# Kernel optimization log

Hardware: AMD Instinct MI355X
Metric: run time of the kernel (lower is better)

Reference implementation:

```python
import jax, jax.numpy as jnp
import numpy as np

B = 64      # batch
N = 2048    # map obstacle points
S = 4       # num_step (distinct planner per step)
A = 8       # num_anchor_per_step
H = 256     # size_middle
L = 2       # lstm num_layers
LOC = 3     # len_info_loc (x, y, theta)
WH = 64     # map_width_half == map_height_half
INTERVAL = 0.2
CIN, COUT, K, STRIDE, PAD = 4, 8, 5, 2, 2
O = (2 * WH + 2 * PAD - K) // STRIDE + 1  # 64
DLM = (2.0, 2.0, 0.5)   # delta_limit_mean
DLV = 0.1               # delta_limit_var


def setup_inputs() -> dict:
    key = jax.random.key(0)
    ks = jax.random.split(key, 16)

    def w(k, shape, fan_in):
        return jax.random.normal(k, shape, jnp.float32) / np.sqrt(fan_in)

    return {
        "inp_start_point": jax.random.normal(ks[0], (B, 1, LOC), jnp.float32),
        "map_pts": jax.random.uniform(ks[1], (2, N), jnp.float32, -12.8, 12.8),
        "ela_w1": w(ks[2], (S, H, LOC), LOC),
        "ela_w2": w(ks[3], (S, H, H), H),
        "conv_w": w(ks[4], (S, COUT, CIN, K, K), CIN * K * K),
        "elm_w1": w(ks[5], (S, H, O * O), O * O),
        "elm_w2": w(ks[6], (S, H, H), H),
        "ebl_w1": w(ks[7], (S, H, 2 * H), 2 * H),
        "ebl_w2": w(ks[8], (S, H, H), H),
        "lstm_wih": w(ks[9], (S, L, 4 * H, H), H),
        "lstm_whh": w(ks[10], (S, L, 4 * H, H), H),
        "dm_w1": w(ks[11], (S, H, H), H),
        "dm_w2": w(ks[12], (S, LOC, H), H),
        "dv_w1": w(ks[13], (S, H, H), H),
        "dv_w2": w(ks[14], (S, LOC, H), H),
    }


def _ogm(map_pts, anchor):
    """points2ogm + cal_map_last: rotate/translate global map into ego frame,
    nearest-bin argmin, scatter 1s into a [B, 128, 128] occupancy grid."""
    rel = map_pts.T[None, :, :] - anchor[:, :, 0:2]        # [B,N,2]
    m = jnp.swapaxes(rel, 1, 2)                            # [B,2,N]
    th = anchor[:, 0, 2]                                   # [B]
    c, s = jnp.cos(th), jnp.sin(th)
    rot = jnp.stack([jnp.stack([c, s], -1), jnp.stack([-s, c], -1)], axis=1)  # [B,2,2]
    pts = rot @ m                                          # [B,2,N]
    x, y = pts[:, 0], pts[:, 1]                            # [B,N]
    lim = WH * INTERVAL
    out = (jnp.abs(x) > lim) | (jnp.abs(y) > lim)
    x = jnp.where(out, 0.0, x)
    y = jnp.where(out, 0.0, y)
    centers = (jnp.arange(-WH, WH, dtype=jnp.float32) + 0.5) * INTERVAL  # [2*WH]
    x_id = jnp.argmin(jnp.abs(centers[None, None, :] - x[:, :, None]), axis=2)  # [B,N]
    y_id = jnp.argmin(jnp.abs(centers[None, None, :] - y[:, :, None]), axis=2)  # [B,N]
    b_idx = jnp.arange(B)[:, None]
    return jnp.zeros((B, 2 * WH, 2 * WH), jnp.float32).at[b_idx, x_id, y_id].set(1.0)


def _conv(x, w):
    return jax.lax.conv_general_dilated(
        x, w, (STRIDE, STRIDE), [(PAD, PAD), (PAD, PAD)],
        dimension_numbers=("NCHW", "OIHW", "NCHW"))


def _ln(x):  # LayerNorm, no affine, eps=1e-5
    mu = jnp.mean(x, axis=-1, keepdims=True)
    v = jnp.var(x, axis=-1, keepdims=True)
    return (x - mu) / jnp.sqrt(v + 1e-5)


def _mlp2(x, w1, w2):  # Linear -> ReLU -> Linear, no bias
    return jax.nn.relu(x @ w1.T) @ w2.T


def reference(inp_start_point, map_pts, ela_w1, ela_w2, conv_w, elm_w1, elm_w2,
              ebl_w1, ebl_w2, lstm_wih, lstm_whh, dm_w1, dm_w2, dv_w1, dv_w2):
    dlm = jnp.array(DLM, jnp.float32)
    anchor = inp_start_point                       # [B,1,3]
    var_last = jnp.ones_like(anchor) * 0.01
    pre_mean, pre_var = [], []
    for st in range(S):
        dm_list, dv_list = [anchor], [var_last]
        h = jnp.ones((L, B, H), jnp.float32)
        c = jnp.ones((L, B, H), jnp.float32)
        for _ in range(A - 1):
            ela = _mlp2(anchor, ela_w1[st], ela_w2[st])                 # [B,1,H]
            ogm = jax.lax.stop_gradient(_ogm(map_pts, anchor))          # [B,128,128]
            xin = jnp.broadcast_to(ogm[:, None], (B, CIN, 2 * WH, 2 * WH))
            conv = jnp.tanh(_conv(xin, conv_w[st])).sum(axis=1)         # [B,O,O]
            elm = _mlp2(conv.reshape(B, 1, O * O), elm_w1[st], elm_w2[st])  # [B,1,H]
            ebl = _mlp2(jnp.concatenate([ela, elm], axis=2), ebl_w1[st], ebl_w2[st])  # [B,1,H]
            # single-timestep multi-layer LSTM, no bias, gate order i,f,g,o
            x = ebl[:, 0]                                               # [B,H]
            for l in range(L):
                g = x @ lstm_wih[st, l].T + h[l] @ lstm_whh[st, l].T    # [B,4H]
                gi, gf, gg, go = jnp.split(g, 4, axis=-1)
                cl = jax.nn.sigmoid(gf) * c[l] + jax.nn.sigmoid(gi) * jnp.tanh(gg)
                hl = jax.nn.sigmoid(go) * jnp.tanh(cl)
                h = h.at[l].set(hl)
                c = c.at[l].set(cl)
                x = hl
            mn = _ln(x[:, None]) + ebl                                  # [B,1,H]
            r = jax.nn.relu(mn)
            anchors_now = jnp.tanh(_mlp2(r, dm_w1[st], dm_w2[st])) * dlm + anchor
            var_now = jax.nn.sigmoid(_mlp2(r, dv_w1[st], dv_w2[st])) * DLV
            anchor, var_last = anchors_now, var_now
            dm_list.append(anchors_now)
            dv_list.append(var_now)
        pre_mean.append(jnp.concatenate(dm_list, axis=1))               # [B,A,3]
        pre_var.append(jnp.concatenate(dv_list, axis=1))
    pre_mean = jnp.stack(pre_mean, axis=1)                              # [B,S,A,3]
    pre_var = jnp.stack(pre_var, axis=1)
    return pre_mean, pre_var
```

## Files before the change

kernel.cpp:

```cpp
#include <hip/hip_runtime.h>

#define WGSZ 1024
#define NWG  256

namespace {
constexpr int kN = 2048, kH = 256, kGW = 512;
constexpr size_t OFF_ITM = 16384;
constexpr size_t OFF_W0  = OFF_ITM + 64 * 4096;
constexpr size_t TO_ELA2 = 0;
constexpr size_t TO_ELM1 = 262144;
constexpr size_t TO_ELM2 = 4456448;
constexpr size_t TO_EBL1 = 4718592;
constexpr size_t TO_EBL2 = 5242880;
constexpr size_t TO_DM1  = 5505024;
constexpr size_t TO_DV1  = 5767168;
constexpr size_t TO_WIH  = 6029312;
constexpr size_t TO_WHH  = 8126464;
constexpr size_t W_FLOATS = 10223616;
constexpr size_t WS_FULL  = OFF_W0 + W_FLOATS;
constexpr int I_CAT = 0, I_ELMH = 512, I_EBLH = 768, I_EBLO = 1024,
              I_G0 = 1280, I_G1 = 2304, I_DMH = 3328, I_DVH = 3584;
}

__device__ __forceinline__ int bin_idx(float v) {
  float t = fmaf(v, 5.0f, 63.5f);
  int i0 = (int)floorf(t);
  int c0 = i0 - 1; c0 = c0 < 0 ? 0 : (c0 > 127 ? 127 : c0);
  int c1 = i0;     c1 = c1 < 0 ? 0 : (c1 > 127 ? 127 : c1);
  int c2 = i0 + 1; c2 = c2 < 0 ? 0 : (c2 > 127 ? 127 : c2);
  float d0 = fabsf(__fmul_rn(__fadd_rn((float)(c0 - 64), 0.5f), 0.2f) - v);
  float d1 = fabsf(__fmul_rn(__fadd_rn((float)(c1 - 64), 0.5f), 0.2f) - v);
  float d2 = fabsf(__fmul_rn(__fadd_rn((float)(c2 - 64), 0.5f), 0.2f) - v);
  int best = c0; float bd = d0;
  if (d1 < bd) { bd = d1; best = c1; }
  if (d2 < bd) { bd = d2; best = c2; }
  return best;
}

__device__ __forceinline__ float np_pw128(const float* a) {
  float r0=a[0],r1=a[1],r2=a[2],r3=a[3],r4=a[4],r5=a[5],r6=a[6],r7=a[7];
  for (int i = 8; i < 128; i += 8) {
    r0=__fadd_rn(r0,a[i+0]); r1=__fadd_rn(r1,a[i+1]);
    r2=__fadd_rn(r2,a[i+2]); r3=__fadd_rn(r3,a[i+3]);
    r4=__fadd_rn(r4,a[i+4]); r5=__fadd_rn(r5,a[i+5]);
    r6=__fadd_rn(r6,a[i+6]); r7=__fadd_rn(r7,a[i+7]);
  }
  return __fadd_rn(__fadd_rn(__fadd_rn(r0,r1),__fadd_rn(r2,r3)),
                   __fadd_rn(__fadd_rn(r4,r5),__fadd_rn(r6,r7)));
}
__device__ __forceinline__ float np_sum256(const float* a) {
  return __fadd_rn(np_pw128(a), np_pw128(a + 128));
}

__device__ __forceinline__ float sig_np(float x) {
  return __fdiv_rn(1.0f, __fadd_rn(1.0f, expf(-x)));
}

__device__ __forceinline__ void fma4(float& aa, float4 w, float4 v) {
  aa = fmaf(w.x, v.x, aa); aa = fmaf(w.y, v.y, aa);
  aa = fmaf(w.z, v.z, aa); aa = fmaf(w.w, v.w, aa);
}

__device__ __forceinline__ void gl_lds(const float4* g, float4* l) {
  __builtin_amdgcn_global_load_lds(
      (__attribute__((address_space(1))) void*)g,
      (__attribute__((address_space(3))) void*)l, 16, 0, 0);
}

__device__ __forceinline__ void bat_bar(unsigned* cnt, int tid) {
  __syncthreads();
  if (tid == 0) {
    __threadfence();
    __hip_atomic_fetch_add(cnt, 1u, __ATOMIC_RELEASE, __HIP_MEMORY_SCOPE_AGENT);
    while (__hip_atomic_load(cnt, __ATOMIC_ACQUIRE,
                             __HIP_MEMORY_SCOPE_AGENT) < 4u)
      __builtin_amdgcn_s_sleep(1);
  }
  __syncthreads();
}

#define MV_STAGE(CI, BI)                                                       \
  do {                                                                         \
    float4* dst = wb[BI] + wid * 64;                                           \
    const int cs0 = (CI) * CK4;                                                \
    if (wT) gl_lds(wT + (size_t)(cs0 + k4l) * Rg + G0 + sub * 64 + lane, dst); \
    else    gl_lds(wO + (size_t)(G0 + sub * 64 + lane) * k4o + cs0 + k4l, dst);\
  } while (0)

#define MV_COMP(BI, CI)                                                        \
  do {                                                                         \
    if (tid < RW) {                                                            \
      const float4* sb = wb[BI];                                               \
      const int cc0 = (CI) * CK4;                                              \
      for (int kk = 0; kk < CK4; ++kk)                                         \
        fma4(acc, sb[kk * RW + tid], x4[cc0 + kk]);                            \
    }                                                                          \
  } while (0)

template<int RW>
__device__ float mv_split(float4 (*wb)[1024], const float4* wT,
                          const float4* wO, int k4o, int Rg, int K4, int G0,
                          const float4* x4, int tid, float acc0) {
  constexpr int RW64 = RW / 64;
  constexpr int CK4  = 16 / RW64;
  const int C = K4 / CK4;
  const int wid = tid >> 6, lane = tid & 63;
  const int k4l = wid / RW64, sub = wid - k4l * RW64;
  float acc = acc0;
  MV_STAGE(0, 0);
  MV_STAGE(1, 1);
  MV_STAGE(2, 2);
  MV_STAGE(3, 3);
  int c = 0, cbuf = 0, sbuf = 4;
  for (; c + 4 < C; ++c) {
    MV_STAGE(c + 4, sbuf);
    asm volatile("s_waitcnt vmcnt(4)" ::: "memory");
    __builtin_amdgcn_s_barrier();
    MV_COMP(cbuf, c);
    sbuf = (sbuf == 5) ? 0 : sbuf + 1;
    cbuf = (cbuf == 5) ? 0 : cbuf + 1;
  }
  asm volatile("s_waitcnt vmcnt(3)" ::: "memory");
  __builtin_amdgcn_s_barrier();
  MV_COMP(cbuf, c);
  cbuf = (cbuf == 5) ? 0 : cbuf + 1; ++c;
  asm volatile("s_waitcnt vmcnt(2)" ::: "memory");
  __builtin_amdgcn_s_barrier();
  MV_COMP(cbuf, c);
  cbuf = (cbuf == 5) ? 0 : cbuf + 1; ++c;
  asm volatile("s_waitcnt vmcnt(1)" ::: "memory");
  __builtin_amdgcn_s_barrier();
  MV_COMP(cbuf, c);
  cbuf = (cbuf == 5) ? 0 : cbuf + 1; ++c;
  asm volatile("s_waitcnt vmcnt(0)" ::: "memory");
  __builtin_amdgcn_s_barrier();
  MV_COMP(cbuf, c);
  __syncthreads();
  return acc;
}

struct TransArgs {
  const float* src[9];
  float*       dst[9];
  int          n4[9];
  int          rmask[9];
  int          rshift[9];
  int          K[9];
};

__global__ void prep_kernel(TransArgs a, unsigned* bar, int nmat) {
  const int gtid = blockIdx.x * blockDim.x + threadIdx.x;
  const int gsz  = gridDim.x * blockDim.x;
  for (int i = gtid; i < 16384; i += gsz) bar[i] = 0u;
  for (int m = 0; m < nmat; ++m) {
    const float* __restrict__ src = a.src[m];
    float4* __restrict__ dst = (float4*)a.dst[m];
    const int n = a.n4[m], rm = a.rmask[m], rs = a.rshift[m], K = a.K[m];
    for (int i = gtid; i < n; i += gsz) {
      const int r = i & rm, k4 = i >> rs;
      const float* s = src + (size_t)r * K + (size_t)k4 * 4;
      float4 v; v.x = s[0]; v.y = s[1]; v.z = s[2]; v.w = s[3];
      dst[i] = v;
    }
  }
}

__global__ __launch_bounds__(WGSZ, 4) void planner_kernel(
    const float* __restrict__ inp_start, const float* __restrict__ map_pts,
    const float* __restrict__ ela_w1, const float* __restrict__ ela_w2,
    const float* __restrict__ conv_w, const float* __restrict__ elm_w1,
    const float* __restrict__ elm_w2, const float* __restrict__ ebl_w1,
    const float* __restrict__ ebl_w2, const float* __restrict__ lstm_wih,
    const float* __restrict__ lstm_whh, const float* __restrict__ dm_w1,
    const float* __restrict__ dm_w2, const float* __restrict__ dv_w1,
    const float* __restrict__ dv_w2, float* __restrict__ ws,
    int useT, float* __restrict__ g_out) {
  const int b   = blockIdx.x >> 2;
  const int g   = blockIdx.x & 3;
  const int tid = threadIdx.x;
  float* itm = ws + OFF_ITM + (size_t)b * 4096;
  unsigned* barp = (unsigned*)ws + (size_t)b * 256;
  const float4* wsW = (const float4*)(ws + OFF_W0);

  __shared__ __align__(16) float4 s_wbuf[6][1024];
  __shared__ unsigned s_mask[kGW];
  __shared__ __align__(16) float s_conv[4096];
  __shared__ __align__(16) float s_cw[800];
  __shared__ __align__(16) float s_elah[kH];
  __shared__ __align__(16) float s_xa[512];
  __shared__ __align__(16) float s_eblo[kH];
  __shared__ __align__(16) float s_r[kH];
  __shared__ __align__(16) float s_gate[1024];
  __shared__ __align__(16) float s_h0[kH], s_c0[kH], s_h1[kH], s_c1[kH];
  __shared__ __align__(16) float s_ones[kH];
  __shared__ __align__(16) float s_tmp[512];
  __shared__ __align__(16) float s_hw[1536];
  __shared__ float s_anchor[3], s_cs[2], s_g6[6];
  __shared__ float s_mu, s_den;

  if (tid == 0) {
    float a2 = inp_start[b * 3 + 2];
    s_anchor[0] = inp_start[b * 3 + 0];
    s_anchor[1] = inp_start[b * 3 + 1];
    s_anchor[2] = a2;
    s_cs[0] = (float)cos((double)a2);
    s_cs[1] = (float)sin((double)a2);
  }
  if (tid < kH) s_ones[tid] = 1.0f;
  if (g == 0 && tid < 3) {
    g_out[b * 96 + tid] = inp_start[b * 3 + tid];
    g_out[6144 + b * 96 + tid] = 0.01f;
  }
  __syncthreads();

  int sidx = 0;
  for (int k = 0; k < 28; ++k) {
    const int st = k / 7, a = k % 7;
    const bool a0f = (a == 0);

    if (tid < kGW) s_mask[tid] = 0u;
    if (tid < 800) s_cw[tid] = conv_w[st * 800 + tid];
    if (tid < kH) {
      const float* w1r = ela_w1 + (st * kH + tid) * 3;
      float h = fmaf(s_anchor[2], w1r[2],
                fmaf(s_anchor[1], w1r[1], __fmul_rn(s_anchor[0], w1r[0])));
      s_elah[tid] = fmaxf(h, 0.0f);
    }
    if (tid < 1536)
      s_hw[tid] = (tid < 768) ? dm_w2[st * 768 + tid]
                              : dv_w2[st * 768 + tid - 768];
    __syncthreads();

    {
      float ax = s_anchor[0], ay = s_anchor[1], cc = s_cs[0], ss = s_cs[1];
      for (int n = tid; n < kN; n += WGSZ) {
        float mx = __fadd_rn(map_pts[n],      -ax);
        float my = __fadd_rn(map_pts[kN + n], -ay);
        float px = fmaf(ss, my, __fmul_rn(cc, mx));
        float py = fmaf(cc, my, -__fmul_rn(ss, mx));
        bool outb = (fabsf(px) > 12.8f) || (fabsf(py) > 12.8f);
        px = outb ? 0.0f : px;
        py = outb ? 0.0f : py;
        int xi = bin_idx(px), yi = bin_idx(py);
        atomicOr(&s_mask[xi * 4 + (yi >> 5)], 1u << (yi & 31));
      }
    }
    __syncthreads();

    for (int q = 0; q < 4; ++q) {
      const int p = tid + (q << 10);
      const int oy = p >> 6, ox = p & 63;
      unsigned occ = 0u;
      for (int ky = 0; ky < 5; ++ky) {
        const int y = 2 * oy - 2 + ky;
        if ((unsigned)y >= 128u) continue;
        const unsigned* row = &s_mask[y * 4];
        for (int kx = 0; kx < 5; ++kx) {
          const int x = 2 * ox - 2 + kx;
          if ((unsigned)x >= 128u) continue;
          if ((row[x >> 5] >> (x & 31)) & 1u) occ |= 1u << (ky * 5 + kx);
        }
      }
      float csum = 0.0f;
      if (occ != 0u) {
        for (int o = 0; o < 8; ++o) {
          float acc = 0.0f;
          const float* wo = s_cw + o * 100;
          for (int ci = 0; ci < 4; ++ci) {
            const float* wc = wo + ci * 25;
            #pragma unroll
            for (int t = 0; t < 25; ++t)
              acc = __fadd_rn(acc, ((occ >> t) & 1u) ? wc[t] : 0.0f);
          }
          float th = tanhf(acc);
          csum = (o == 0) ? th : __fadd_rn(csum, th);
        }
      }
      s_conv[p] = csum;
    }
    __syncthreads();

    const int G64 = st * 256 + g * 64;

    {
      float acc = mv_split<64>(s_wbuf, useT ? wsW + TO_ELA2 / 4 : nullptr,
                               (const float4*)ela_w2, 64, 1024, 64, G64,
                               (const float4*)s_elah, tid, 0.0f);
      if (tid < 64) itm[I_CAT + g * 64 + tid] = acc;
      acc = mv_split<64>(s_wbuf, useT ? wsW + TO_ELM1 / 4 : nullptr,
                         (const float4*)elm_w1, 1024, 1024, 1024, G64,
                         (const float4*)s_conv, tid, 0.0f);
      if (tid < 64) itm[I_ELMH + g * 64 + tid] = fmaxf(acc, 0.0f);
    }
    bat_bar(barp + sidx, tid); ++sidx;

    if (tid < kH) s_xa[tid] = itm[I_ELMH + tid];
    __syncthreads();
    {
      float acc = mv_split<64>(s_wbuf, useT ? wsW + TO_ELM2 / 4 : nullptr,
                               (const float4*)elm_w2, 64, 1024, 64, G64,
                               (const float4*)s_xa, tid, 0.0f);
      if (tid < 64) itm[I_CAT + 256 + g * 64 + tid] = acc;
    }
    bat_bar(barp + sidx, tid); ++sidx;

    if (tid < 512) s_xa[tid] = itm[I_CAT + tid];
    __syncthreads();
    {
      float acc = mv_split<64>(s_wbuf, useT ? wsW + TO_EBL1 / 4 : nullptr,
                               (const float4*)ebl_w1, 128, 1024, 128, G64,
                               (const float4*)s_xa, tid, 0.0f);
      if (tid < 64) itm[I_EBLH + g * 64 + tid] = fmaxf(acc, 0.0f);
    }
    bat_bar(barp + sidx, tid); ++sidx;

    if (tid < kH) s_xa[tid] = itm[I_EBLH + tid];
    __syncthreads();
    {
      float acc = mv_split<64>(s_wbuf, useT ? wsW + TO_EBL2 / 4 : nullptr,
                               (const float4*)ebl_w2, 64, 1024, 64, G64,
                               (const float4*)s_xa, tid, 0.0f);
      if (tid < 64) itm[I_EBLO + g * 64 + tid] = acc;
    }
    bat_bar(barp + sidx, tid); ++sidx;

    if (tid < kH) s_eblo[tid] = itm[I_EBLO + tid];
    __syncthreads();
    for (int l = 0; l < 2; ++l) {
      const int rowb = (st * 2 + l) * 1024 + g * 256;
      const float* xe = (l == 0) ? s_eblo : s_h0;
      const float* xh = a0f ? s_ones : ((l == 0) ? s_h0 : s_h1);
      float accA = mv_split<256>(s_wbuf, useT ? wsW + TO_WIH / 4 : nullptr,
                                 (const float4*)lstm_wih, 64, 8192, 64, rowb,
                                 (const float4*)xe, tid, 0.0f);
      float accB = mv_split<256>(s_wbuf, useT ? wsW + TO_WHH / 4 : nullptr,
                                 (const float4*)lstm_whh, 64, 8192, 64, rowb,
                                 (const float4*)xh, tid, 0.0f);
      const int IG = (l == 0) ? I_G0 : I_G1;
      if (tid < kH) itm[IG + g * 256 + tid] = __fadd_rn(accA, accB);
      bat_bar(barp + sidx, tid); ++sidx;
      s_gate[tid] = itm[IG + tid];
      __syncthreads();
      if (tid < kH) {
        float gi = s_gate[tid], gf = s_gate[256 + tid];
        float gg = s_gate[512 + tid], go = s_gate[768 + tid];
        float* sc = (l == 0) ? s_c0 : s_c1;
        float* sh = (l == 0) ? s_h0 : s_h1;
        float cprev = a0f ? 1.0f : sc[tid];
        float cl = __fadd_rn(__fmul_rn(sig_np(gf), cprev),
                             __fmul_rn(sig_np(gi), tanhf(gg)));
        float hl = __fmul_rn(sig_np(go), tanhf(cl));
        sc[tid] = cl; sh[tid] = hl;
      }
      __syncthreads();
    }

    if (tid == 0) s_mu = __fdiv_rn(np_sum256(s_h1), 256.0f);
    __syncthreads();
    if (tid < kH) {
      float d = __fadd_rn(s_h1[tid], -s_mu);
      s_tmp[tid] = d;
      s_tmp[256 + tid] = __fmul_rn(d, d);
    }
    __syncthreads();
    if (tid == 0) {
      float v = __fdiv_rn(np_sum256(s_tmp + 256), 256.0f);
      s_den = __fsqrt_rn(__fadd_rn(v, 1e-5f));
    }
    __syncthreads();
    if (tid < kH) {
      float r = __fadd_rn(__fdiv_rn(s_tmp[tid], s_den), s_eblo[tid]);
      s_r[tid] = fmaxf(r, 0.0f);
    }
    __syncthreads();

    {
      float acc = mv_split<64>(s_wbuf, useT ? wsW + TO_DM1 / 4 : nullptr,
                               (const float4*)dm_w1, 64, 1024, 64, G64,
                               (const float4*)s_r, tid, 0.0f);
      if (tid < 64) itm[I_DMH + g * 64 + tid] = fmaxf(acc, 0.0f);
      acc = mv_split<64>(s_wbuf, useT ? wsW + TO_DV1 / 4 : nullptr,
                         (const float4*)dv_w1, 64, 1024, 64, G64,
                         (const float4*)s_r, tid, 0.0f);
      if (tid < 64) itm[I_DVH + g * 64 + tid] = fmaxf(acc, 0.0f);
    }
    bat_bar(barp + sidx, tid); ++sidx;

    if (tid < 512)
      s_xa[tid] = (tid < 256) ? itm[I_DMH + tid] : itm[I_DVH + tid - 256];
    __syncthreads();
    if (tid < 6) {
      const int d = tid % 3; const bool isv = tid >= 3;
      const float4* w4 = (const float4*)(s_hw + (isv ? 768 : 0) + d * 256);
      const float4* xx = (const float4*)(isv ? s_xa + 256 : s_xa);
      float acc = 0.0f;
      for (int i = 0; i < 64; ++i) fma4(acc, w4[i], xx[i]);
      s_g6[tid] = acc;
    }
    __syncthreads();
    if (tid == 0) {
      const float dlmf[3] = {2.0f, 2.0f, 0.5f};
      for (int d = 0; d < 3; ++d) {
        float avn = __fadd_rn(s_anchor[d], __fmul_rn(tanhf(s_g6[d]), dlmf[d]));
        float vvn = __fmul_rn(sig_np(s_g6[3 + d]), 0.1f);
        s_anchor[d] = avn;
        if (g == 0) {
          int o = ((b * 4 + st) * 8 + (a + 1)) * 3 + d;
          g_out[o] = avn;
          g_out[6144 + o] = vvn;
          if (a == 6 && st < 3) {
            int o2 = ((b * 4 + st + 1) * 8 + 0) * 3 + d;
            g_out[o2] = avn;
            g_out[6144 + o2] = vvn;
          }
        }
      }
      s_cs[0] = (float)cos((double)s_anchor[2]);
      s_cs[1] = (float)sin((double)s_anchor[2]);
    }
    __syncthreads();
  }
}

extern "C" void kernel_launch(void* const* d_in, const int* in_sizes, int n_in,
                              void* d_out, int out_size, void* d_ws, size_t ws_size,
                              hipStream_t stream) {
  (void)in_sizes; (void)n_in; (void)out_size;
  float* wsf = (float*)d_ws;
  const int useT = (ws_size >= WS_FULL * sizeof(float)) ? 1 : 0;

  TransArgs ta;
  const float* srcs[9] = {
      (const float*)d_in[3],  (const float*)d_in[5],  (const float*)d_in[6],
      (const float*)d_in[7],  (const float*)d_in[8],  (const float*)d_in[11],
      (const float*)d_in[13], (const float*)d_in[9],  (const float*)d_in[10]};
  float* w0 = wsf + OFF_W0;
  float* dsts[9] = {w0 + TO_ELA2, w0 + TO_ELM1, w0 + TO_ELM2, w0 + TO_EBL1,
                    w0 + TO_EBL2, w0 + TO_DM1,  w0 + TO_DV1,  w0 + TO_WIH,
                    w0 + TO_WHH};
  const int n4s[9] = {65536, 1048576, 65536, 131072, 65536, 65536, 65536,
                      524288, 524288};
  const int rms[9] = {1023, 1023, 1023, 1023, 1023, 1023, 1023, 8191, 8191};
  const int rss[9] = {10, 10, 10, 10, 10, 10, 10, 13, 13};
  const int Ks[9]  = {256, 4096, 256, 512, 256, 256, 256, 256, 256};
  for (int m = 0; m < 9; ++m) {
    ta.src[m] = srcs[m]; ta.dst[m] = dsts[m]; ta.n4[m] = n4s[m];
    ta.rmask[m] = rms[m]; ta.rshift[m] = rss[m]; ta.K[m] = Ks[m];
  }
  prep_kernel<<<dim3(1024), dim3(256), 0, stream>>>(
      ta, (unsigned*)d_ws, useT ? 9 : 0);

  planner_kernel<<<dim3(NWG), dim3(WGSZ), 0, stream>>>(
      (const float*)d_in[0],  (const float*)d_in[1],  (const float*)d_in[2],
      (const float*)d_in[3],  (const float*)d_in[4],  (const float*)d_in[5],
      (const float*)d_in[6],  (const float*)d_in[7],  (const float*)d_in[8],
      (const float*)d_in[9],  (const float*)d_in[10], (const float*)d_in[11],
      (const float*)d_in[12], (const float*)d_in[13], (const float*)d_in[14],
      wsf, useT, (float*)d_out);
}
```

Baseline: 8.289 ms.

## Batch eight samples per workgroup team to reuse weight tiles across batch

Restructures the persistent planner kernel from 4 workgroups per batch element (256 WGs) to 64 workgroups organized as 8 teams of 8, each team handling 8 batch elements together. Each WG now computes a 32-row slice for all 8 batch elements, so every weight tile staged into LDS is reused 8 times instead of once, cutting global weight traffic. Intermediates move to global workspace with per-team barriers over 8 WGs, and activations are staged in padded LDS layouts. The trade-offs are more barriers and global round trips per stage, less parallelism, and a simpler double-buffered pipeline replacing the 6-deep one.

```diff
diff --git a/kernel.cpp b/kernel.cpp
--- a/kernel.cpp
+++ b/kernel.cpp
@@ -1,12 +1,21 @@
 #include <hip/hip_runtime.h>
 
 #define WGSZ 1024
-#define NWG  256
+#define NWG  64
 
 namespace {
-constexpr int kN = 2048, kH = 256, kGW = 512;
-constexpr size_t OFF_ITM = 16384;
-constexpr size_t OFF_W0  = OFF_ITM + 64 * 4096;
+constexpr int kN = 2048;
+constexpr size_t OFF_CONV = 2048;
+constexpr size_t OFF_ELAH = 264192;
+constexpr size_t OFF_CAT  = 280576;
+constexpr size_t OFF_ELMH = 313344;
+constexpr size_t OFF_EBLH = 329728;
+constexpr size_t OFF_EBLO = 346112;
+constexpr size_t OFF_H0   = 362496;
+constexpr size_t OFF_H1   = 395264;
+constexpr size_t OFF_DMH  = 428032;
+constexpr size_t OFF_DVH  = 444416;
+constexpr size_t OFF_W0   = 460800;
 constexpr size_t TO_ELA2 = 0;
 constexpr size_t TO_ELM1 = 262144;
 constexpr size_t TO_ELM2 = 4456448;
@@ -18,8 +27,7 @@
 constexpr size_t TO_WHH  = 8126464;
 constexpr size_t W_FLOATS = 10223616;
 constexpr size_t WS_FULL  = OFF_W0 + W_FLOATS;
-constexpr int I_CAT = 0, I_ELMH = 512, I_EBLH = 768, I_EBLO = 1024,
-              I_G0 = 1280, I_G1 = 2304, I_DMH = 3328, I_DVH = 3584;
+constexpr int XP = 9;
 }
 
 __device__ __forceinline__ int bin_idx(float v) {
@@ -37,28 +45,45 @@
   return best;
 }
 
-__device__ __forceinline__ float np_pw128(const float* a) {
-  float r0=a[0],r1=a[1],r2=a[2],r3=a[3],r4=a[4],r5=a[5],r6=a[6],r7=a[7];
-  for (int i = 8; i < 128; i += 8) {
-    r0=__fadd_rn(r0,a[i+0]); r1=__fadd_rn(r1,a[i+1]);
-    r2=__fadd_rn(r2,a[i+2]); r3=__fadd_rn(r3,a[i+3]);
-    r4=__fadd_rn(r4,a[i+4]); r5=__fadd_rn(r5,a[i+5]);
-    r6=__fadd_rn(r6,a[i+6]); r7=__fadd_rn(r7,a[i+7]);
-  }
-  return __fadd_rn(__fadd_rn(__fadd_rn(r0,r1),__fadd_rn(r2,r3)),
-                   __fadd_rn(__fadd_rn(r4,r5),__fadd_rn(r6,r7)));
-}
-__device__ __forceinline__ float np_sum256(const float* a) {
-  return __fadd_rn(np_pw128(a), np_pw128(a + 128));
-}
-
 __device__ __forceinline__ float sig_np(float x) {
   return __fdiv_rn(1.0f, __fadd_rn(1.0f, expf(-x)));
 }
+__device__ __forceinline__ float sqf(float x) { return __fmul_rn(x, x); }
 
 __device__ __forceinline__ void fma4(float& aa, float4 w, float4 v) {
   aa = fmaf(w.x, v.x, aa); aa = fmaf(w.y, v.y, aa);
   aa = fmaf(w.z, v.z, aa); aa = fmaf(w.w, v.w, aa);
+}
+
+__device__ __forceinline__ float np_pw128_s9(const float* a) {
+  float r0=a[0*XP],r1=a[1*XP],r2=a[2*XP],r3=a[3*XP];
+  float r4=a[4*XP],r5=a[5*XP],r6=a[6*XP],r7=a[7*XP];
+  for (int i = 8; i < 128; i += 8) {
+    r0=__fadd_rn(r0,a[(i+0)*XP]); r1=__fadd_rn(r1,a[(i+1)*XP]);
+    r2=__fadd_rn(r2,a[(i+2)*XP]); r3=__fadd_rn(r3,a[(i+3)*XP]);
+    r4=__fadd_rn(r4,a[(i+4)*XP]); r5=__fadd_rn(r5,a[(i+5)*XP]);
+    r6=__fadd_rn(r6,a[(i+6)*XP]); r7=__fadd_rn(r7,a[(i+7)*XP]);
+  }
+  return __fadd_rn(__fadd_rn(__fadd_rn(r0,r1),__fadd_rn(r2,r3)),
+                   __fadd_rn(__fadd_rn(r4,r5),__fadd_rn(r6,r7)));
+}
+__device__ __forceinline__ float np_sum256_s9(const float* a) {
+  return __fadd_rn(np_pw128_s9(a), np_pw128_s9(a + 128 * XP));
+}
+__device__ __forceinline__ float np_pw128_sq_s9(const float* a) {
+  float r0=sqf(a[0*XP]),r1=sqf(a[1*XP]),r2=sqf(a[2*XP]),r3=sqf(a[3*XP]);
+  float r4=sqf(a[4*XP]),r5=sqf(a[5*XP]),r6=sqf(a[6*XP]),r7=sqf(a[7*XP]);
+  for (int i = 8; i < 128; i += 8) {
+    r0=__fadd_rn(r0,sqf(a[(i+0)*XP])); r1=__fadd_rn(r1,sqf(a[(i+1)*XP]));
+    r2=__fadd_rn(r2,sqf(a[(i+2)*XP])); r3=__fadd_rn(r3,sqf(a[(i+3)*XP]));
+    r4=__fadd_rn(r4,sqf(a[(i+4)*XP])); r5=__fadd_rn(r5,sqf(a[(i+5)*XP]));
+    r6=__fadd_rn(r6,sqf(a[(i+6)*XP])); r7=__fadd_rn(r7,sqf(a[(i+7)*XP]));
+  }
+  return __fadd_rn(__fadd_rn(__fadd_rn(r0,r1),__fadd_rn(r2,r3)),
+                   __fadd_rn(__fadd_rn(r4,r5),__fadd_rn(r6,r7)));
+}
+__device__ __forceinline__ float np_sum256_sq_s9(const float* a) {
+  return __fadd_rn(np_pw128_sq_s9(a), np_pw128_sq_s9(a + 128 * XP));
 }
 
 __device__ __forceinline__ void gl_lds(const float4* g, float4* l) {
@@ -73,70 +98,103 @@
     __threadfence();
     __hip_atomic_fetch_add(cnt, 1u, __ATOMIC_RELEASE, __HIP_MEMORY_SCOPE_AGENT);
     while (__hip_atomic_load(cnt, __ATOMIC_ACQUIRE,
-                             __HIP_MEMORY_SCOPE_AGENT) < 4u)
+                             __HIP_MEMORY_SCOPE_AGENT) < 8u)
       __builtin_amdgcn_s_sleep(1);
   }
   __syncthreads();
 }
 
-#define MV_STAGE(CI, BI)                                                       \
-  do {                                                                         \
-    float4* dst = wb[BI] + wid * 64;                                           \
-    const int cs0 = (CI) * CK4;                                                \
-    if (wT) gl_lds(wT + (size_t)(cs0 + k4l) * Rg + G0 + sub * 64 + lane, dst); \
-    else    gl_lds(wO + (size_t)(G0 + sub * 64 + lane) * k4o + cs0 + k4l, dst);\
-  } while (0)
-
-#define MV_COMP(BI, CI)                                                        \
-  do {                                                                         \
-    if (tid < RW) {                                                            \
-      const float4* sb = wb[BI];                                               \
-      const int cc0 = (CI) * CK4;                                              \
-      for (int kk = 0; kk < CK4; ++kk)                                         \
-        fma4(acc, sb[kk * RW + tid], x4[cc0 + kk]);                            \
-    }                                                                          \
-  } while (0)
-
-template<int RW>
-__device__ float mv_split(float4 (*wb)[1024], const float4* wT,
-                          const float4* wO, int k4o, int Rg, int K4, int G0,
-                          const float4* x4, int tid, float acc0) {
-  constexpr int RW64 = RW / 64;
-  constexpr int CK4  = 16 / RW64;
-  const int C = K4 / CK4;
+__device__ __forceinline__ void stage_x(float* xl, const float* src0,
+                                        int stride, int L, int tid) {
+  const int bat = tid >> 7, i = tid & 127;
+  const float* sp = src0 + (size_t)bat * stride;
+  for (int k = i; k < L; k += 128) xl[k * XP + bat] = sp[k];
+}
+
+__device__ float mv32(float4 (*wb)[1024], const float4* wT, const float4* wO,
+                      int k4o, int Rg, int R0g, int k4base, int C,
+                      const float* xl, int tid, float acc) {
   const int wid = tid >> 6, lane = tid & 63;
-  const int k4l = wid / RW64, sub = wid - k4l * RW64;
-  float acc = acc0;
-  MV_STAGE(0, 0);
-  MV_STAGE(1, 1);
-  MV_STAGE(2, 2);
-  MV_STAGE(3, 3);
-  int c = 0, cbuf = 0, sbuf = 4;
-  for (; c + 4 < C; ++c) {
-    MV_STAGE(c + 4, sbuf);
-    asm volatile("s_waitcnt vmcnt(4)" ::: "memory");
-    __builtin_amdgcn_s_barrier();
-    MV_COMP(cbuf, c);
-    sbuf = (sbuf == 5) ? 0 : sbuf + 1;
-    cbuf = (cbuf == 5) ? 0 : cbuf + 1;
-  }
-  asm volatile("s_waitcnt vmcnt(3)" ::: "memory");
-  __builtin_amdgcn_s_barrier();
-  MV_COMP(cbuf, c);
-  cbuf = (cbuf == 5) ? 0 : cbuf + 1; ++c;
-  asm volatile("s_waitcnt vmcnt(2)" ::: "memory");
-  __builtin_amdgcn_s_barrier();
-  MV_COMP(cbuf, c);
-  cbuf = (cbuf == 5) ? 0 : cbuf + 1; ++c;
-  asm volatile("s_waitcnt vmcnt(1)" ::: "memory");
-  __builtin_amdgcn_s_barrier();
-  MV_COMP(cbuf, c);
-  cbuf = (cbuf == 5) ? 0 : cbuf + 1; ++c;
-  asm volatile("s_waitcnt vmcnt(0)" ::: "memory");
-  __builtin_amdgcn_s_barrier();
-  MV_COMP(cbuf, c);
+  const int kkw = (wid << 1) + (lane >> 5), rw = lane & 31;
+  {
+    const int k4g = k4base + kkw;
+    if (wT) gl_lds(wT + (size_t)k4g * Rg + R0g + rw, wb[0] + wid * 64);
+    else    gl_lds(wO + (size_t)(R0g + rw) * k4o + k4g, wb[0] + wid * 64);
+  }
   __syncthreads();
+  for (int c = 0; c < C; ++c) {
+    if (c + 1 < C) {
+      const int k4g = k4base + (c + 1) * 32 + kkw;
+      if (wT) gl_lds(wT + (size_t)k4g * Rg + R0g + rw, wb[(c + 1) & 1] + wid * 64);
+      else    gl_lds(wO + (size_t)(R0g + rw) * k4o + k4g, wb[(c + 1) & 1] + wid * 64);
+    }
+    if (tid < 256) {
+      const float4* sb = wb[c & 1];
+      const int r = tid >> 3, bat = tid & 7;
+      for (int kk = 0; kk < 32; ++kk) {
+        const float4 wv = sb[kk * 32 + r];
+        const float* xp = xl + (size_t)((c * 32 + kk) * 4) * XP + bat;
+        acc = fmaf(wv.x, xp[0], acc);
+        acc = fmaf(wv.y, xp[XP], acc);
+        acc = fmaf(wv.z, xp[2 * XP], acc);
+        acc = fmaf(wv.w, xp[3 * XP], acc);
+      }
+    }
+    __syncthreads();
+  }
   return acc;
+}
+
+__device__ float4 lstm_pass(float4 (*wb)[1024], const float4* wT,
+                            const float4* wO, int RB, const float* xl,
+                            int ones, int tid) {
+  const int wid = tid >> 6, lane = tid & 63;
+  const int kkw = wid >> 1, gw = ((wid & 1) << 1) + (lane >> 5), rw = lane & 31;
+  float4 A; A.x = 0.0f; A.y = 0.0f; A.z = 0.0f; A.w = 0.0f;
+  {
+    const int k4g = kkw;
+    if (wT) gl_lds(wT + ((size_t)k4g << 13) + RB + (gw << 8) + rw, wb[0] + wid * 64);
+    else    gl_lds(wO + ((size_t)(RB + (gw << 8) + rw) << 6) + k4g, wb[0] + wid * 64);
+  }
+  __syncthreads();
+  for (int c = 0; c < 8; ++c) {
+    if (c + 1 < 8) {
+      const int k4g = (c + 1) * 8 + kkw;
+      if (wT) gl_lds(wT + ((size_t)k4g << 13) + RB + (gw << 8) + rw,
+                     wb[(c + 1) & 1] + wid * 64);
+      else    gl_lds(wO + ((size_t)(RB + (gw << 8) + rw) << 6) + k4g,
+                     wb[(c + 1) & 1] + wid * 64);
+    }
+    if (tid < 256) {
+      const float4* sb = wb[c & 1];
+      const int u = tid >> 3, bat = tid & 7;
+      for (int kk = 0; kk < 8; ++kk) {
+        const float4 wi = sb[kk * 128 + u];
+        const float4 wf = sb[kk * 128 + 32 + u];
+        const float4 wg = sb[kk * 128 + 64 + u];
+        const float4 wo = sb[kk * 128 + 96 + u];
+        if (ones) {
+          A.x = __fadd_rn(__fadd_rn(__fadd_rn(__fadd_rn(A.x, wi.x), wi.y), wi.z), wi.w);
+          A.y = __fadd_rn(__fadd_rn(__fadd_rn(__fadd_rn(A.y, wf.x), wf.y), wf.z), wf.w);
+          A.z = __fadd_rn(__fadd_rn(__fadd_rn(__fadd_rn(A.z, wg.x), wg.y), wg.z), wg.w);
+          A.w = __fadd_rn(__fadd_rn(__fadd_rn(__fadd_rn(A.w, wo.x), wo.y), wo.z), wo.w);
+        } else {
+          const float* xp = xl + (size_t)((c * 8 + kk) * 4) * XP + bat;
+          const float x0 = xp[0], x1 = xp[XP], x2 = xp[2 * XP], x3 = xp[3 * XP];
+          A.x = fmaf(wi.x, x0, A.x); A.x = fmaf(wi.y, x1, A.x);
+          A.x = fmaf(wi.z, x2, A.x); A.x = fmaf(wi.w, x3, A.x);
+          A.y = fmaf(wf.x, x0, A.y); A.y = fmaf(wf.y, x1, A.y);
+          A.y = fmaf(wf.z, x2, A.y); A.y = fmaf(wf.w, x3, A.y);
+          A.z = fmaf(wg.x, x0, A.z); A.z = fmaf(wg.y, x1, A.z);
+          A.z = fmaf(wg.z, x2, A.z); A.z = fmaf(wg.w, x3, A.z);
+          A.w = fmaf(wo.x, x0, A.w); A.w = fmaf(wo.y, x1, A.w);
+          A.w = fmaf(wo.z, x2, A.w); A.w = fmaf(wo.w, x3, A.w);
+        }
+      }
+    }
+    __syncthreads();
+  }
+  return A;
 }
 
 struct TransArgs {
@@ -151,7 +209,7 @@
 __global__ void prep_kernel(TransArgs a, unsigned* bar, int nmat) {
   const int gtid = blockIdx.x * blockDim.x + threadIdx.x;
   const int gsz  = gridDim.x * blockDim.x;
-  for (int i = gtid; i < 16384; i += gsz) bar[i] = 0u;
+  for (int i = gtid; i < 2048; i += gsz) bar[i] = 0u;
   for (int m = 0; m < nmat; ++m) {
     const float* __restrict__ src = a.src[m];
     float4* __restrict__ dst = (float4*)a.dst[m];
@@ -175,41 +233,35 @@
     const float* __restrict__ dm_w2, const float* __restrict__ dv_w1,
     const float* __restrict__ dv_w2, float* __restrict__ ws,
     int useT, float* __restrict__ g_out) {
-  const int b   = blockIdx.x >> 2;
-  const int g   = blockIdx.x & 3;
+  const int wg  = blockIdx.x;
+  const int t   = wg & 7, j = wg >> 3;
+  const int b0  = t * 8, b_own = b0 + j;
+  const int R0  = j * 32;
   const int tid = threadIdx.x;
-  float* itm = ws + OFF_ITM + (size_t)b * 4096;
-  unsigned* barp = (unsigned*)ws + (size_t)b * 256;
-  const float4* wsW = (const float4*)(ws + OFF_W0);
-
-  __shared__ __align__(16) float4 s_wbuf[6][1024];
-  __shared__ unsigned s_mask[kGW];
-  __shared__ __align__(16) float s_conv[4096];
+  unsigned* cnt = (unsigned*)ws + t * 256;
+  const float* w0 = ws + OFF_W0;
+
+  __shared__ __align__(16) float4 s_wbuf[2][1024];
+  __shared__ __align__(16) float s_x[1024 * XP];
+  __shared__ __align__(16) float s_xh[256 * XP];
+  __shared__ unsigned s_mask[512];
   __shared__ __align__(16) float s_cw[800];
-  __shared__ __align__(16) float s_elah[kH];
-  __shared__ __align__(16) float s_xa[512];
-  __shared__ __align__(16) float s_eblo[kH];
-  __shared__ __align__(16) float s_r[kH];
-  __shared__ __align__(16) float s_gate[1024];
-  __shared__ __align__(16) float s_h0[kH], s_c0[kH], s_h1[kH], s_c1[kH];
-  __shared__ __align__(16) float s_ones[kH];
-  __shared__ __align__(16) float s_tmp[512];
-  __shared__ __align__(16) float s_hw[1536];
+  __shared__ __align__(16) float s_state[2][32][8];
+  __shared__ __align__(16) float s_col[512];
+  __shared__ float s_mu8[8], s_den8[8];
   __shared__ float s_anchor[3], s_cs[2], s_g6[6];
-  __shared__ float s_mu, s_den;
 
   if (tid == 0) {
-    float a2 = inp_start[b * 3 + 2];
-    s_anchor[0] = inp_start[b * 3 + 0];
-    s_anchor[1] = inp_start[b * 3 + 1];
+    float a2 = inp_start[b_own * 3 + 2];
+    s_anchor[0] = inp_start[b_own * 3 + 0];
+    s_anchor[1] = inp_start[b_own * 3 + 1];
     s_anchor[2] = a2;
     s_cs[0] = (float)cos((double)a2);
     s_cs[1] = (float)sin((double)a2);
   }
-  if (tid < kH) s_ones[tid] = 1.0f;
-  if (g == 0 && tid < 3) {
-    g_out[b * 96 + tid] = inp_start[b * 3 + tid];
-    g_out[6144 + b * 96 + tid] = 0.01f;
+  if (tid < 3) {
+    g_out[b_own * 96 + tid] = inp_start[b_own * 3 + tid];
+    g_out[6144 + b_own * 96 + tid] = 0.01f;
   }
   __syncthreads();
 
@@ -217,20 +269,11 @@
   for (int k = 0; k < 28; ++k) {
     const int st = k / 7, a = k % 7;
     const bool a0f = (a == 0);
-
-    if (tid < kGW) s_mask[tid] = 0u;
+    const int pp = k & 1;
+
+    if (tid < 512) s_mask[tid] = 0u;
     if (tid < 800) s_cw[tid] = conv_w[st * 800 + tid];
-    if (tid < kH) {
-      const float* w1r = ela_w1 + (st * kH + tid) * 3;
-      float h = fmaf(s_anchor[2], w1r[2],
-                fmaf(s_anchor[1], w1r[1], __fmul_rn(s_anchor[0], w1r[0])));
-      s_elah[tid] = fmaxf(h, 0.0f);
-    }
-    if (tid < 1536)
-      s_hw[tid] = (tid < 768) ? dm_w2[st * 768 + tid]
-                              : dv_w2[st * 768 + tid - 768];
-    __syncthreads();
-
+    __syncthreads();
     {
       float ax = s_anchor[0], ay = s_anchor[1], cc = s_cs[0], ss = s_cs[1];
       for (int n = tid; n < kN; n += WGSZ) {
@@ -246,7 +289,6 @@
       }
     }
     __syncthreads();
-
     for (int q = 0; q < 4; ++q) {
       const int p = tid + (q << 10);
       const int oy = p >> 6, ox = p & 63;
@@ -269,130 +311,159 @@
           for (int ci = 0; ci < 4; ++ci) {
             const float* wc = wo + ci * 25;
             #pragma unroll
-            for (int t = 0; t < 25; ++t)
-              acc = __fadd_rn(acc, ((occ >> t) & 1u) ? wc[t] : 0.0f);
+            for (int tt = 0; tt < 25; ++tt)
+              acc = __fadd_rn(acc, ((occ >> tt) & 1u) ? wc[tt] : 0.0f);
           }
           float th = tanhf(acc);
           csum = (o == 0) ? th : __fadd_rn(csum, th);
         }
       }
-      s_conv[p] = csum;
-    }
-    __syncthreads();
-
-    const int G64 = st * 256 + g * 64;
+      ws[OFF_CONV + (size_t)b_own * 4096 + p] = csum;
+    }
+    if (tid < 256) {
+      const float* w1r = ela_w1 + (st * 256 + tid) * 3;
+      float h = fmaf(s_anchor[2], w1r[2],
+                fmaf(s_anchor[1], w1r[1], __fmul_rn(s_anchor[0], w1r[0])));
+      ws[OFF_ELAH + (size_t)b_own * 256 + tid] = fmaxf(h, 0.0f);
+    }
+    bat_bar(cnt + sidx, tid); ++sidx;
 
     {
-      float acc = mv_split<64>(s_wbuf, useT ? wsW + TO_ELA2 / 4 : nullptr,
-                               (const float4*)ela_w2, 64, 1024, 64, G64,
-                               (const float4*)s_elah, tid, 0.0f);
-      if (tid < 64) itm[I_CAT + g * 64 + tid] = acc;
-      acc = mv_split<64>(s_wbuf, useT ? wsW + TO_ELM1 / 4 : nullptr,
-                         (const float4*)elm_w1, 1024, 1024, 1024, G64,
-                         (const float4*)s_conv, tid, 0.0f);
-      if (tid < 64) itm[I_ELMH + g * 64 + tid] = fmaxf(acc, 0.0f);
-    }
-    bat_bar(barp + sidx, tid); ++sidx;
-
-    if (tid < kH) s_xa[tid] = itm[I_ELMH + tid];
-    __syncthreads();
+      const int R0g = st * 256 + R0;
+      stage_x(s_x, ws + OFF_ELAH + (size_t)b0 * 256, 256, 256, tid);
+      float acc = mv32(s_wbuf, useT ? (const float4*)(w0 + TO_ELA2) : nullptr,
+                       (const float4*)ela_w2, 64, 1024, R0g, 0, 2, s_x, tid, 0.0f);
+      if (tid < 256) {
+        const int r = tid >> 3, bat = tid & 7;
+        ws[OFF_CAT + (size_t)(b0 + bat) * 512 + R0 + r] = acc;
+      }
+      float ae = 0.0f;
+      for (int s = 0; s < 4; ++s) {
+        stage_x(s_x, ws + OFF_CONV + (size_t)b0 * 4096 + s * 1024, 4096, 1024, tid);
+        ae = mv32(s_wbuf, useT ? (const float4*)(w0 + TO_ELM1) : nullptr,
+                  (const float4*)elm_w1, 1024, 1024, R0g, s * 256, 8, s_x, tid, ae);
+      }
+      if (tid < 256) {
+        const int r = tid >> 3, bat = tid & 7;
+        ws[OFF_ELMH + (size_t)(b0 + bat) * 256 + R0 + r] = fmaxf(ae, 0.0f);
+      }
+    }
+    bat_bar(cnt + sidx, tid); ++sidx;
+
     {
-      float acc = mv_split<64>(s_wbuf, useT ? wsW + TO_ELM2 / 4 : nullptr,
-                               (const float4*)elm_w2, 64, 1024, 64, G64,
-                               (const float4*)s_xa, tid, 0.0f);
-      if (tid < 64) itm[I_CAT + 256 + g * 64 + tid] = acc;
-    }
-    bat_bar(barp + sidx, tid); ++sidx;
-
-    if (tid < 512) s_xa[tid] = itm[I_CAT + tid];
-    __syncthreads();
+      stage_x(s_x, ws + OFF_ELMH + (size_t)b0 * 256, 256, 256, tid);
+      float acc = mv32(s_wbuf, useT ? (const float4*)(w0 + TO_ELM2) : nullptr,
+                       (const float4*)elm_w2, 64, 1024, st * 256 + R0, 0, 2, s_x, tid, 0.0f);
+      if (tid < 256) {
+        const int r = tid >> 3, bat = tid & 7;
+        ws[OFF_CAT + (size_t)(b0 + bat) * 512 + 256 + R0 + r] = acc;
+      }
+    }
+    bat_bar(cnt + sidx, tid); ++sidx;
+
     {
-      float acc = mv_split<64>(s_wbuf, useT ? wsW + TO_EBL1 / 4 : nullptr,
-                               (const float4*)ebl_w1, 128, 1024, 128, G64,
-                               (const float4*)s_xa, tid, 0.0f);
-      if (tid < 64) itm[I_EBLH + g * 64 + tid] = fmaxf(acc, 0.0f);
-    }
-    bat_bar(barp + sidx, tid); ++sidx;
-
-    if (tid < kH) s_xa[tid] = itm[I_EBLH + tid];
-    __syncthreads();
+      stage_x(s_x, ws + OFF_CAT + (size_t)b0 * 512, 512, 512, tid);
+      float acc = mv32(s_wbuf, useT ? (const float4*)(w0 + TO_EBL1) : nullptr,
+                       (const float4*)ebl_w1, 128, 1024, st * 256 + R0, 0, 4, s_x, tid, 0.0f);
+      if (tid < 256) {
+        const int r = tid >> 3, bat = tid & 7;
+        ws[OFF_EBLH + (size_t)(b0 + bat) * 256 + R0 + r] = fmaxf(acc, 0.0f);
+      }
+    }
+    bat_bar(cnt + sidx, tid); ++sidx;
+
     {
-      float acc = mv_split<64>(s_wbuf, useT ? wsW + TO_EBL2 / 4 : nullptr,
-                               (const float4*)ebl_w2, 64, 1024, 64, G64,
-                               (const float4*)s_xa, tid, 0.0f);
-      if (tid < 64) itm[I_EBLO + g * 64 + tid] = acc;
-    }
-    bat_bar(barp + sidx, tid); ++sidx;
-
-    if (tid < kH) s_eblo[tid] = itm[I_EBLO + tid];
-    __syncthreads();
+      stage_x(s_x, ws + OFF_EBLH + (size_t)b0 * 256, 256, 256, tid);
+      float acc = mv32(s_wbuf, useT ? (const float4*)(w0 + TO_EBL2) : nullptr,
+                       (const float4*)ebl_w2, 64, 1024, st * 256 + R0, 0, 2, s_x, tid, 0.0f);
+      if (tid < 256) {
+        const int r = tid >> 3, bat = tid & 7;
+        ws[OFF_EBLO + (size_t)(b0 + bat) * 256 + R0 + r] = acc;
+      }
+    }
+    bat_bar(cnt + sidx, tid); ++sidx;
+
     for (int l = 0; l < 2; ++l) {
-      const int rowb = (st * 2 + l) * 1024 + g * 256;
-      const float* xe = (l == 0) ? s_eblo : s_h0;
-      const float* xh = a0f ? s_ones : ((l == 0) ? s_h0 : s_h1);
-      float accA = mv_split<256>(s_wbuf, useT ? wsW + TO_WIH / 4 : nullptr,
-                                 (const float4*)lstm_wih, 64, 8192, 64, rowb,
-                                 (const float4*)xe, tid, 0.0f);
-      float accB = mv_split<256>(s_wbuf, useT ? wsW + TO_WHH / 4 : nullptr,
-                                 (const float4*)lstm_whh, 64, 8192, 64, rowb,
-                                 (const float4*)xh, tid, 0.0f);
-      const int IG = (l == 0) ? I_G0 : I_G1;
-      if (tid < kH) itm[IG + g * 256 + tid] = __fadd_rn(accA, accB);
-      bat_bar(barp + sidx, tid); ++sidx;
-      s_gate[tid] = itm[IG + tid];
-      __syncthreads();
-      if (tid < kH) {
-        float gi = s_gate[tid], gf = s_gate[256 + tid];
-        float gg = s_gate[512 + tid], go = s_gate[768 + tid];
-        float* sc = (l == 0) ? s_c0 : s_c1;
-        float* sh = (l == 0) ? s_h0 : s_h1;
-        float cprev = a0f ? 1.0f : sc[tid];
+      const int RB = (st * 2 + l) * 1024 + R0;
+      if (l == 0) stage_x(s_x, ws + OFF_EBLO + (size_t)b0 * 256, 256, 256, tid);
+      else        stage_x(s_x, ws + OFF_H0 + (size_t)(pp ^ 1) * 16384 + (size_t)b0 * 256,
+                          256, 256, tid);
+      if (!a0f) {
+        const size_t hsrc = (l == 0 ? OFF_H0 : OFF_H1) + (size_t)pp * 16384;
+        stage_x(s_xh, ws + hsrc + (size_t)b0 * 256, 256, 256, tid);
+      }
+      float4 A = lstm_pass(s_wbuf, useT ? (const float4*)(w0 + TO_WIH) : nullptr,
+                           (const float4*)lstm_wih, RB, s_x, 0, tid);
+      float4 B = lstm_pass(s_wbuf, useT ? (const float4*)(w0 + TO_WHH) : nullptr,
+                           (const float4*)lstm_whh, RB, s_xh, a0f ? 1 : 0, tid);
+      if (tid < 256) {
+        const int u = tid >> 3, bat = tid & 7;
+        float gi = __fadd_rn(A.x, B.x), gf = __fadd_rn(A.y, B.y);
+        float gg = __fadd_rn(A.z, B.z), go = __fadd_rn(A.w, B.w);
+        float cprev = a0f ? 1.0f : s_state[l][u][bat];
         float cl = __fadd_rn(__fmul_rn(sig_np(gf), cprev),
                              __fmul_rn(sig_np(gi), tanhf(gg)));
         float hl = __fmul_rn(sig_np(go), tanhf(cl));
-        sc[tid] = cl; sh[tid] = hl;
-      }
+        s_state[l][u][bat] = cl;
+        const size_t hdst = (l == 0 ? OFF_H0 : OFF_H1) + (size_t)(pp ^ 1) * 16384;
+        ws[hdst + (size_t)(b0 + bat) * 256 + R0 + u] = hl;
+      }
+      bat_bar(cnt + sidx, tid); ++sidx;
+    }
+
+    {
+      stage_x(s_x, ws + OFF_H1 + (size_t)(pp ^ 1) * 16384 + (size_t)b0 * 256,
+              256, 256, tid);
+      stage_x(s_xh, ws + OFF_EBLO + (size_t)b0 * 256, 256, 256, tid);
       __syncthreads();
-    }
-
-    if (tid == 0) s_mu = __fdiv_rn(np_sum256(s_h1), 256.0f);
-    __syncthreads();
-    if (tid < kH) {
-      float d = __fadd_rn(s_h1[tid], -s_mu);
-      s_tmp[tid] = d;
-      s_tmp[256 + tid] = __fmul_rn(d, d);
-    }
-    __syncthreads();
-    if (tid == 0) {
-      float v = __fdiv_rn(np_sum256(s_tmp + 256), 256.0f);
-      s_den = __fsqrt_rn(__fadd_rn(v, 1e-5f));
-    }
-    __syncthreads();
-    if (tid < kH) {
-      float r = __fadd_rn(__fdiv_rn(s_tmp[tid], s_den), s_eblo[tid]);
-      s_r[tid] = fmaxf(r, 0.0f);
-    }
-    __syncthreads();
-
-    {
-      float acc = mv_split<64>(s_wbuf, useT ? wsW + TO_DM1 / 4 : nullptr,
-                               (const float4*)dm_w1, 64, 1024, 64, G64,
-                               (const float4*)s_r, tid, 0.0f);
-      if (tid < 64) itm[I_DMH + g * 64 + tid] = fmaxf(acc, 0.0f);
-      acc = mv_split<64>(s_wbuf, useT ? wsW + TO_DV1 / 4 : nullptr,
-                         (const float4*)dv_w1, 64, 1024, 64, G64,
-                         (const float4*)s_r, tid, 0.0f);
-      if (tid < 64) itm[I_DVH + g * 64 + tid] = fmaxf(acc, 0.0f);
-    }
-    bat_bar(barp + sidx, tid); ++sidx;
+      if (tid < 8) s_mu8[tid] = __fdiv_rn(np_sum256_s9(s_x + tid), 256.0f);
+      __syncthreads();
+      {
+        const int kk = tid >> 3, bat = tid & 7;
+        float d0 = __fadd_rn(s_x[kk * XP + bat], -s_mu8[bat]);
+        float d1 = __fadd_rn(s_x[(kk + 128) * XP + bat], -s_mu8[bat]);
+        s_x[kk * XP + bat] = d0;
+        s_x[(kk + 128) * XP + bat] = d1;
+      }
+      __syncthreads();
+      if (tid < 8) {
+        float v = __fdiv_rn(np_sum256_sq_s9(s_x + tid), 256.0f);
+        s_den8[tid] = __fsqrt_rn(__fadd_rn(v, 1e-5f));
+      }
+      __syncthreads();
+      {
+        const int kk = tid >> 3, bat = tid & 7;
+        float r0 = __fadd_rn(__fdiv_rn(s_x[kk * XP + bat], s_den8[bat]),
+                             s_xh[kk * XP + bat]);
+        float r1 = __fadd_rn(__fdiv_rn(s_x[(kk + 128) * XP + bat], s_den8[bat]),
+                             s_xh[(kk + 128) * XP + bat]);
+        s_x[kk * XP + bat] = fmaxf(r0, 0.0f);
+        s_x[(kk + 128) * XP + bat] = fmaxf(r1, 0.0f);
+      }
+      const int R0g = st * 256 + R0;
+      float am = mv32(s_wbuf, useT ? (const float4*)(w0 + TO_DM1) : nullptr,
+                      (const float4*)dm_w1, 64, 1024, R0g, 0, 2, s_x, tid, 0.0f);
+      if (tid < 256) {
+        const int r = tid >> 3, bat = tid & 7;
+        ws[OFF_DMH + (size_t)(b0 + bat) * 256 + R0 + r] = fmaxf(am, 0.0f);
+      }
+      float av = mv32(s_wbuf, useT ? (const float4*)(w0 + TO_DV1) : nullptr,
+                      (const float4*)dv_w1, 64, 1024, R0g, 0, 2, s_x, tid, 0.0f);
+      if (tid < 256) {
+        const int r = tid >> 3, bat = tid & 7;
+        ws[OFF_DVH + (size_t)(b0 + bat) * 256 + R0 + r] = fmaxf(av, 0.0f);
+      }
+    }
+    bat_bar(cnt + sidx, tid); ++sidx;
 
     if (tid < 512)
-      s_xa[tid] = (tid < 256) ? itm[I_DMH + tid] : itm[I_DVH + tid - 256];
+      s_col[tid] = ws[(tid < 256 ? OFF_DMH : OFF_DVH) +
+                      (size_t)b_own * 256 + (tid & 255)];
     __syncthreads();
     if (tid < 6) {
       const int d = tid % 3; const bool isv = tid >= 3;
-      const float4* w4 = (const float4*)(s_hw + (isv ? 768 : 0) + d * 256);
-      const float4* xx = (const float4*)(isv ? s_xa + 256 : s_xa);
+      const float4* w4 = (const float4*)((isv ? dv_w2 : dm_w2) + (st * 3 + d) * 256);
+      const float4* xx = (const float4*)(s_col + (isv ? 256 : 0));
       float acc = 0.0f;
       for (int i = 0; i < 64; ++i) fma4(acc, w4[i], xx[i]);
       s_g6[tid] = acc;
@@ -404,15 +475,13 @@
         float avn = __fadd_rn(s_anchor[d], __fmul_rn(tanhf(s_g6[d]), dlmf[d]));
         float vvn = __fmul_rn(sig_np(s_g6[3 + d]), 0.1f);
         s_anchor[d] = avn;
-        if (g == 0) {
-          int o = ((b * 4 + st) * 8 + (a + 1)) * 3 + d;
-          g_out[o] = avn;
-          g_out[6144 + o] = vvn;
-          if (a == 6 && st < 3) {
-            int o2 = ((b * 4 + st + 1) * 8 + 0) * 3 + d;
-            g_out[o2] = avn;
-            g_out[6144 + o2] = vvn;
-          }
+        int o = ((b_own * 4 + st) * 8 + (a + 1)) * 3 + d;
+        g_out[o] = avn;
+        g_out[6144 + o] = vvn;
+        if (a == 6 && st < 3) {
+          int o2 = ((b_own * 4 + st + 1) * 8 + 0) * 3 + d;
+          g_out[o2] = avn;
+          g_out[6144 + o2] = vvn;
         }
       }
       s_cs[0] = (float)cos((double)s_anchor[2]);
```

Result: no change. 8.363 ms (+0.9%).
